# Performance work log

Measured on AMD Instinct MI355X. Metric: run time of the kernel, lower is better.

## Reference

```python
import jax, jax.numpy as jnp
import numpy as np

B, T, C = 4, 1024, 512
H, HD = 8, 64
NE, K = 8, 2
FF = 4 * C


def setup_inputs() -> dict:
    key = jax.random.key(0)
    ks = jax.random.split(key, 16)
    s = 0.02
    return {
        "x": jax.random.normal(ks[0], (B, T, C), jnp.float32),
        "ln1_g": jnp.ones((C,), jnp.float32),
        "ln1_b": jnp.zeros((C,), jnp.float32),
        "ln2_g": jnp.ones((C,), jnp.float32),
        "ln2_b": jnp.zeros((C,), jnp.float32),
        "Wq": jax.random.normal(ks[1], (H, C, HD), jnp.float32) * s,
        "Wk": jax.random.normal(ks[2], (H, C, HD), jnp.float32) * s,
        "Wv": jax.random.normal(ks[3], (H, C, HD), jnp.float32) * s,
        "Wp": jax.random.normal(ks[4], (H * HD, C), jnp.float32) * s,
        "bp": jnp.zeros((C,), jnp.float32),
        "Wr": jax.random.normal(ks[5], (C, NE), jnp.float32) * s,
        "br": jnp.zeros((NE,), jnp.float32),
        "W1": jax.random.normal(ks[6], (NE, C, FF), jnp.float32) * s,
        "b1": jnp.zeros((NE, FF), jnp.float32),
        "W2": jax.random.normal(ks[7], (NE, FF, C), jnp.float32) * s,
        "b2": jnp.zeros((NE, C), jnp.float32),
    }


def _ln(x, g, b, eps=1e-5):
    mu = jnp.mean(x, axis=-1, keepdims=True)
    var = jnp.var(x, axis=-1, keepdims=True)
    return (x - mu) * jax.lax.rsqrt(var + eps) * g + b


def reference(x, ln1_g, ln1_b, ln2_g, ln2_b, Wq, Wk, Wv, Wp, bp, Wr, br, W1, b1, W2, b2):
    # --- multi-head causal attention (all heads stacked) ---
    h = _ln(x, ln1_g, ln1_b)
    q = jnp.einsum("btc,hcd->bhtd", h, Wq)
    k = jnp.einsum("btc,hcd->bhtd", h, Wk)
    v = jnp.einsum("btc,hcd->bhtd", h, Wv)
    wei = jnp.einsum("bhtd,bhsd->bhts", q, k) / np.sqrt(HD).astype(np.float32)
    causal = jnp.tril(jnp.ones((T, T), bool))
    wei = jnp.where(causal, wei, -jnp.inf)
    wei = jax.nn.softmax(wei, axis=-1)
    attn = jnp.einsum("bhts,bhsd->bhtd", wei, v)  # [B,H,T,HD]
    attn = attn.transpose(0, 2, 1, 3).reshape(B, T, H * HD)
    x2 = x + attn @ Wp + bp

    # --- SparseMoE: dense all-experts compute, masked top-k combine ---
    h2 = _ln(x2, ln2_g, ln2_b)
    scores = h2 @ Wr + br  # [B,T,NE]
    topk_scores, indices = jax.lax.top_k(scores, K)
    # scatter top-k scores into zeros (rest stays 0), then softmax over experts
    mask = jnp.sum(jax.nn.one_hot(indices, NE, dtype=scores.dtype) * topk_scores[..., None], axis=-2)
    router = jax.nn.softmax(mask, axis=-1)  # [B,T,NE]
    hid = jax.nn.relu(jnp.einsum("btc,ecf->btef", h2, W1) + b1)  # [B,T,NE,FF]
    eo = jnp.einsum("btef,efc->btec", hid, W2) + b2  # [B,T,NE,C]
    moe = jnp.einsum("bte,btec->btc", router, eo)
    return x2 + moe
```

## Files before the change

kernel.cpp:

```cpp
#include <hip/hip_runtime.h>


typedef unsigned short u16;
typedef __attribute__((ext_vector_type(8))) short s16x8;
typedef __attribute__((ext_vector_type(4))) float f32x4;

__device__ __forceinline__ u16 f2bf(float f) {
  union { float f; unsigned u; } v; v.f = f;
  unsigned r = v.u + 0x7fffu + ((v.u >> 16) & 1u);
  return (u16)(r >> 16);
}
__device__ __forceinline__ float bf2f(u16 h) {
  union { unsigned u; float f; } v; v.u = ((unsigned)h) << 16;
  return v.f;
}

#define GLDS16(g, s) __builtin_amdgcn_global_load_lds( \
    (const __attribute__((address_space(1))) void*)(g), \
    (__attribute__((address_space(3))) void*)(s), 16, 0, 0)

#define MFMA16(a, b, c) __builtin_amdgcn_mfma_f32_16x16x32_bf16((a), (b), (c), 0, 0, 0)

__global__ __launch_bounds__(256) void transpose_k(
    const float* __restrict__ in, u16* __restrict__ out,
    int R, int C, long long ibs, long long obs, float scale)
{
  __shared__ float tile[32][33];
  in  += (long long)blockIdx.z * ibs;
  out += (long long)blockIdx.z * obs;
  const int c0 = blockIdx.x * 32, r0 = blockIdx.y * 32;
  const int tx = threadIdx.x, ty = threadIdx.y;
  #pragma unroll
  for (int i = 0; i < 4; ++i)
    tile[ty + i*8][tx] = in[(size_t)(r0 + ty + i*8) * C + c0 + tx];
  __syncthreads();
  #pragma unroll
  for (int i = 0; i < 4; ++i)
    out[(size_t)(c0 + ty + i*8) * R + r0 + tx] = f2bf(tile[tx][ty + i*8] * scale);
}

__global__ __launch_bounds__(256) void transW_k(
    const float* __restrict__ W1, const float* __restrict__ W2,
    u16* __restrict__ w1t, u16* __restrict__ w2f)
{
  __shared__ float tile[32][33];
  const int z = blockIdx.z;
  const int tx = threadIdx.x, ty = threadIdx.y;
  if (z < 8) {
    const float* in = W1 + (size_t)z * 512 * 2048;
    u16* out = w1t + (size_t)z * 2048 * 512;
    const int c0 = blockIdx.x * 32, r0 = blockIdx.y * 32;
    #pragma unroll
    for (int i = 0; i < 4; ++i)
      tile[ty + i*8][tx] = in[(size_t)(r0 + ty + i*8) * 2048 + c0 + tx];
    __syncthreads();
    #pragma unroll
    for (int i = 0; i < 4; ++i)
      out[(size_t)(c0 + ty + i*8) * 512 + r0 + tx] = f2bf(tile[tx][ty + i*8]);
  } else {
    const int e = z - 8;
    const float* in = W2 + (size_t)e * 2048 * 512;
    const int r0 = blockIdx.x * 32, c0 = blockIdx.y * 32;
    #pragma unroll
    for (int i = 0; i < 4; ++i)
      tile[ty + i*8][tx] = in[(size_t)(r0 + ty + i*8) * 512 + c0 + tx];
    __syncthreads();
    #pragma unroll
    for (int i = 0; i < 4; ++i)
      w2f[(size_t)(c0 + ty + i*8) * 16384 + e*2048 + r0 + tx] = f2bf(tile[tx][ty + i*8]);
  }
}

__global__ __launch_bounds__(256) void transqkv_k(
    const float* __restrict__ Wq, const float* __restrict__ Wk,
    const float* __restrict__ Wv, const float* __restrict__ Wp,
    u16* __restrict__ oqkv, u16* __restrict__ owp)
{
  __shared__ float tile[32][33];
  const int z = blockIdx.z;
  const int tx = threadIdx.x, ty = threadIdx.y;
  if (z < 24) {
    const int which = z >> 3, head = z & 7;
    const float* in = (which == 0 ? Wq : (which == 1 ? Wk : Wv)) + (size_t)head * 512 * 64;
    u16* o = oqkv + (size_t)which * 512 * 512 + (size_t)head * 64 * 512;
    const float scale = (which == 0) ? 0.125f : 1.f;
    const int c0 = blockIdx.x * 32, r0 = blockIdx.y * 32;
    #pragma unroll
    for (int i = 0; i < 4; ++i)
      tile[ty + i*8][tx] = in[(size_t)(r0 + ty + i*8) * 64 + c0 + tx];
    __syncthreads();
    #pragma unroll
    for (int i = 0; i < 4; ++i)
      o[(size_t)(c0 + ty + i*8) * 512 + r0 + tx] = f2bf(tile[tx][ty + i*8] * scale);
  } else {
    const int zz = z - 24;
    const int c0 = (zz * 2 + blockIdx.x) * 32;
    const int r0 = blockIdx.y * 32;
    #pragma unroll
    for (int i = 0; i < 4; ++i)
      tile[ty + i*8][tx] = Wp[(size_t)(r0 + ty + i*8) * 512 + c0 + tx];
    __syncthreads();
    #pragma unroll
    for (int i = 0; i < 4; ++i)
      owp[(size_t)(c0 + ty + i*8) * 512 + r0 + tx] = f2bf(tile[tx][ty + i*8]);
  }
}

__global__ __launch_bounds__(256) void vtrans_k(
    const u16* __restrict__ qkv, u16* __restrict__ vt)
{
  __shared__ u16 tile[32][33];
  const int bh = blockIdx.z, b = bh >> 3, h = bh & 7;
  const int t0 = blockIdx.x * 32, d0 = blockIdx.y * 32;
  const int tx = threadIdx.x, ty = threadIdx.y;
  #pragma unroll
  for (int i = 0; i < 4; ++i)
    tile[ty + i*8][tx] = qkv[(size_t)(b*1024 + t0 + ty + i*8) * 1536 + 1024 + h*64 + d0 + tx];
  __syncthreads();
  #pragma unroll
  for (int i = 0; i < 4; ++i)
    vt[(size_t)bh*65536 + (size_t)(d0 + ty + i*8) * 1024 + t0 + tx] = tile[tx][ty + i*8];
}

__global__ __launch_bounds__(256) void ln_k(
    const float* __restrict__ x, const float* __restrict__ g,
    const float* __restrict__ b, u16* __restrict__ o)
{
  const int row = blockIdx.x, t = threadIdx.x;
  const float* xr = x + (size_t)row * 512;
  const float a0 = xr[t], a1 = xr[t + 256];
  float s = a0 + a1, ss = a0*a0 + a1*a1;
  #pragma unroll
  for (int off = 1; off < 64; off <<= 1) {
    s  += __shfl_xor(s, off);
    ss += __shfl_xor(ss, off);
  }
  __shared__ float rs[4], rq[4];
  const int w = t >> 6;
  if ((t & 63) == 0) { rs[w] = s; rq[w] = ss; }
  __syncthreads();
  s  = rs[0] + rs[1] + rs[2] + rs[3];
  ss = rq[0] + rq[1] + rq[2] + rq[3];
  const float mu = s * (1.f/512.f);
  const float var = ss * (1.f/512.f) - mu*mu;
  const float rstd = rsqrtf(var + 1e-5f);
  o[(size_t)row*512 + t]       = f2bf((a0 - mu) * rstd * g[t]     + b[t]);
  o[(size_t)row*512 + t + 256] = f2bf((a1 - mu) * rstd * g[t+256] + b[t+256]);
}

template<int BN, int EPI>
__global__ __launch_bounds__(256) void gemm2p(
    const u16* __restrict__ A, const u16* __restrict__ Bt,
    int M, int N, int K, int lda, int ldb,
    u16* __restrict__ obf, float* __restrict__ oa,
    const float* __restrict__ bias, const float* __restrict__ extra, int e0)
{
  constexpr int NB = BN / 32;
  constexpr int SB = BN / 32;
  __shared__ u16 Asm[2][128*64];
  __shared__ u16 Bsm[2][BN*64];
  const int t = threadIdx.x, l = t & 63;
  const int wid = t >> 6, wr = wid >> 1, wc = wid & 1;
  const int lrow = l & 15, lhi = l >> 4;
  const int m0 = blockIdx.x * 128, n0 = blockIdx.y * BN;

  const f32x4 z4 = {0.f, 0.f, 0.f, 0.f};
  f32x4 acc[4][NB];
  #pragma unroll
  for (int i = 0; i < 4; ++i)
    #pragma unroll
    for (int j = 0; j < NB; ++j) acc[i][j] = z4;

  const int csw = ((t & 7) ^ ((t >> 3) & 7)) * 8;
  const u16* ga = A  + (size_t)(m0 + (t >> 3)) * lda + csw;
  const u16* gb = Bt + (size_t)(n0 + (t >> 3)) * ldb + csw;

#define STG2(buf, k0) do { \
    _Pragma("unroll") \
    for (int i = 0; i < 4; ++i) \
      GLDS16(ga + (size_t)(i*32)*lda + (k0), (char*)Asm[buf] + i*4096 + t*16); \
    _Pragma("unroll") \
    for (int i = 0; i < SB; ++i) \
      GLDS16(gb + (size_t)(i*32)*ldb + (k0), (char*)Bsm[buf] + i*4096 + t*16); \
  } while (0)

#define RD2(Ls, row, kb) (*(const s16x8*)((const char*)(Ls) + (row)*128 + ((kb) ^ (((row)&7)<<4))))

  const int NT = K >> 6;
  STG2(0, 0);
  for (int tt = 0; tt < NT; ++tt) {
    if (tt + 1 < NT) {
      STG2((tt + 1) & 1, (tt + 1) * 64);
      if constexpr (BN == 128)     asm volatile("s_waitcnt vmcnt(8)" ::: "memory");
      else if constexpr (BN == 96) asm volatile("s_waitcnt vmcnt(7)" ::: "memory");
      else                         asm volatile("s_waitcnt vmcnt(6)" ::: "memory");
    } else {
      asm volatile("s_waitcnt vmcnt(0)" ::: "memory");
    }
    __builtin_amdgcn_sched_barrier(0);
    __builtin_amdgcn_s_barrier();
    const u16* As = Asm[tt & 1];
    const u16* Bs = Bsm[tt & 1];
    #pragma unroll
    for (int kh = 0; kh < 2; ++kh) {
      s16x8 af[4], bfr[NB];
      #pragma unroll
      for (int i = 0; i < 4; ++i)
        af[i]  = RD2(As, wr*64 + i*16 + lrow, kh*64 + lhi*16);
      #pragma unroll
      for (int j = 0; j < NB; ++j)
        bfr[j] = RD2(Bs, wc*(BN/2) + j*16 + lrow, kh*64 + lhi*16);
      #pragma unroll
      for (int i = 0; i < 4; ++i)
        #pragma unroll
        for (int j = 0; j < NB; ++j)
          acc[i][j] = MFMA16(af[i], bfr[j], acc[i][j]);
    }
    __builtin_amdgcn_s_barrier();
    __builtin_amdgcn_sched_barrier(0);
  }
#undef STG2
#undef RD2

  #pragma unroll
  for (int i = 0; i < 4; ++i) {
    const int rbase = m0 + wr*64 + i*16 + lhi*4;
    #pragma unroll
    for (int j = 0; j < NB; ++j) {
      const int col = n0 + wc*(BN/2) + j*16 + lrow;
      #pragma unroll
      for (int rr = 0; rr < 4; ++rr) {
        const int row = rbase + rr;
        const float v = acc[i][j][rr];
        if (EPI == 0) {
          obf[(size_t)row*N + col] = f2bf(v);
        } else if (EPI == 1) {
          const float r = extra[(size_t)row*8 + e0 + (col >> 11)];
          obf[(size_t)row*N + col] = f2bf(fmaxf(v + bias[col], 0.f) * r);
        } else {
          oa[(size_t)row*N + col] = v + bias[col] + extra[(size_t)row*N + col];
        }
      }
    }
  }
}

template<int NKT, int EPI>
__global__ __launch_bounds__(512, 2) void gemm8p(
    const u16* __restrict__ A, const u16* __restrict__ Bt,
    int lda, int ldb,
    u16* __restrict__ obf,
    const float* __restrict__ bias, const float* __restrict__ rout)
{
  __shared__ u16 Lds[2][2][256*64];
  const int t = threadIdx.x, l = t & 63;
  const int wid = t >> 6, wm = wid >> 2, wn = wid & 3;
  const int lrow = l & 15, lhi = l >> 4;

  int m0, n0, zz = 0;
  {
    const int bid = blockIdx.x;
    const int r = bid & 7, k = bid >> 3;
    if (EPI == 1) {
      m0 = (k >> 3) * 256; n0 = (r * 8 + (k & 7)) * 256;
    } else if (EPI == 2) {
      n0 = (r * 8 + (k & 7)) * 256; m0 = (k >> 3) * 256;
    } else if (EPI == 4) {
      zz = r*4 + (k & 3);
      const int mn = k >> 2;
      m0 = (mn >> 1) * 256; n0 = (mn & 1) * 256;
    } else {
      zz = r*2 + (k & 1);
      const int mn = k >> 1;
      m0 = (mn >> 1) * 256; n0 = (mn & 1) * 256;
    }
  }
  constexpr int KCH = (EPI == 4) ? 512 : 1024;
  const u16* Ab = A  + (size_t)m0 * lda + ((EPI == 4 || EPI == 5) ? zz * KCH : 0);
  const u16* Bb = Bt + (size_t)n0 * ldb + ((EPI == 4 || EPI == 5) ? zz * KCH : 0);

  const int tr = t >> 3;
  const int sc = ((t & 7) ^ (tr & 7)) * 8;

#define STGU(bf, kt, op_, u4_) do { \
    const u16* s_ = (op_) ? Bb : Ab; \
    const int ld_ = (op_) ? ldb : lda; \
    GLDS16(s_ + (size_t)((u4_)*64 + tr) * ld_ + (size_t)(kt)*64 + sc, \
           (char*)&Lds[bf][op_][0] + (u4_)*8192 + t*16); \
  } while (0)

#define RD(Ls, row, kb) (*(const s16x8*)((const char*)(Ls) + (row)*128 + ((kb) ^ (((row)&7)<<4))))

  f32x4 acc[8][4];
  const f32x4 z4 = {0.f, 0.f, 0.f, 0.f};
  #pragma unroll
  for (int i = 0; i < 8; ++i)
    #pragma unroll
    for (int j = 0; j < 4; ++j) acc[i][j] = z4;

  #pragma unroll
  for (int u = 0; u < 4; ++u) STGU(0, 0, 0, u);
  #pragma unroll
  for (int u = 0; u < 4; ++u) STGU(0, 0, 1, u);
  if (NKT > 1) {
    #pragma unroll
    for (int u = 0; u < 4; ++u) STGU(1, 1, 1, u);
    asm volatile("s_waitcnt vmcnt(4)" ::: "memory");
  } else {
    asm volatile("s_waitcnt vmcnt(0)" ::: "memory");
  }
  __builtin_amdgcn_sched_barrier(0);
  __builtin_amdgcn_s_barrier();

  s16x8 frA[2][4], frB[2][4];
  #pragma unroll 2
  for (int X = 0; X < NKT; ++X) {
    const u16* As = &Lds[X & 1][0][0];
    const u16* Bs = &Lds[X & 1][1][0];
    #pragma unroll
    for (int kk = 0; kk < 2; ++kk) {
      #pragma unroll
      for (int nf = 0; nf < 4; ++nf)
        frB[kk][nf] = RD(Bs, wn*64 + nf*16 + lrow, kk*64 + lhi*16);
      #pragma unroll
      for (int mf = 0; mf < 4; ++mf)
        frA[kk][mf] = RD(As, wm*128 + mf*16 + lrow, kk*64 + lhi*16);
    }
    if (X + 1 < NKT) {
      #pragma unroll
      for (int u = 0; u < 4; ++u) STGU((X + 1) & 1, X + 1, 0, u);
    }
    __builtin_amdgcn_s_barrier();
    asm volatile("s_waitcnt lgkmcnt(0)" ::: "memory");
    __builtin_amdgcn_sched_barrier(0);
    __builtin_amdgcn_s_setprio(1);
    #pragma unroll
    for (int kk = 0; kk < 2; ++kk)
      #pragma unroll
      for (int mf = 0; mf < 4; ++mf)
        #pragma unroll
        for (int nf = 0; nf < 4; ++nf)
          acc[mf][nf] = MFMA16(frA[kk][mf], frB[kk][nf], acc[mf][nf]);
    __builtin_amdgcn_s_setprio(0);
    __builtin_amdgcn_s_barrier();
    #pragma unroll
    for (int kk = 0; kk < 2; ++kk)
      #pragma unroll
      for (int mf = 0; mf < 4; ++mf)
        frA[kk][mf] = RD(As, wm*128 + 64 + mf*16 + lrow, kk*64 + lhi*16);
    if (X + 2 < NKT) {
      #pragma unroll
      for (int u = 0; u < 4; ++u) STGU(X & 1, X + 2, 1, u);
    }
    __builtin_amdgcn_s_barrier();
    asm volatile("s_waitcnt lgkmcnt(0)" ::: "memory");
    __builtin_amdgcn_sched_barrier(0);
    __builtin_amdgcn_s_setprio(1);
    #pragma unroll
    for (int kk = 0; kk < 2; ++kk)
      #pragma unroll
      for (int mf = 0; mf < 4; ++mf)
        #pragma unroll
        for (int nf = 0; nf < 4; ++nf)
          acc[4 + mf][nf] = MFMA16(frA[kk][mf], frB[kk][nf], acc[4 + mf][nf]);
    __builtin_amdgcn_s_setprio(0);
    if (X + 1 < NKT) {
      if (X + 2 < NKT) asm volatile("s_waitcnt vmcnt(4)" ::: "memory");
      else             asm volatile("s_waitcnt vmcnt(0)" ::: "memory");
      __builtin_amdgcn_sched_barrier(0);
    }
    __builtin_amdgcn_s_barrier();
  }
#undef STGU
#undef RD

  constexpr size_t PSTRIDE = (EPI == 4) ? (size_t)1024*512 : (size_t)2048*512;
  u16* outp = (EPI == 4 || EPI == 5) ? obf + (size_t)zz * PSTRIDE : obf;
  #pragma unroll
  for (int mf = 0; mf < 8; ++mf) {
    const int rbase = m0 + wm*128 + mf*16 + lhi*4;
    #pragma unroll
    for (int nf = 0; nf < 4; ++nf) {
      const int col = n0 + wn*64 + nf*16 + lrow;
      #pragma unroll
      for (int rr = 0; rr < 4; ++rr) {
        const int row = rbase + rr;
        float v = acc[mf][nf][rr];
        if (EPI == 1 || EPI == 2) {
          const float r = rout[(size_t)row*8 + (col >> 11)];
          outp[(size_t)row*16384 + col] = f2bf(fmaxf(v + bias[col], 0.f) * r);
        } else {
          outp[(size_t)row*512 + col] = f2bf(v);
        }
      }
    }
  }
}

template<int Z>
__global__ __launch_bounds__(256) void combineZ_k(
    float* __restrict__ outq, const u16* __restrict__ P, size_t pstride,
    const float* __restrict__ routq, const float* __restrict__ b2)
{
  const int row = blockIdx.x, t = threadIdx.x;
  const int c = t * 2;
  float r[8];
  #pragma unroll
  for (int e = 0; e < 8; ++e) r[e] = routq[(size_t)row*8 + e];
  float v0 = outq[(size_t)row*512 + c];
  float v1 = outq[(size_t)row*512 + c + 1];
  #pragma unroll
  for (int z = 0; z < Z; ++z) {
    const unsigned pv = *(const unsigned*)(P + (size_t)z*pstride + (size_t)row*512 + c);
    v0 += bf2f((u16)(pv & 0xffffu));
    v1 += bf2f((u16)(pv >> 16));
  }
  #pragma unroll
  for (int e = 0; e < 8; ++e) {
    v0 += r[e] * b2[(size_t)e*512 + c];
    v1 += r[e] * b2[(size_t)e*512 + c + 1];
  }
  outq[(size_t)row*512 + c]     = v0;
  outq[(size_t)row*512 + c + 1] = v1;
}

__global__ __launch_bounds__(256) void gemm2_k(
    const u16* __restrict__ hid, const u16* __restrict__ w2t,
    u16* __restrict__ P, int e0, int accum)
{
  __shared__ u16 Asm[128*64];
  __shared__ u16 Bsm[64*64];
  const int t = threadIdx.x;
  const int l = t & 63;
  const int wid = t >> 6, wr = wid >> 1, wc = wid & 1;
  const int lrow = l & 15, lhi = l >> 4;
  const int m0 = blockIdx.x * 128, n0 = blockIdx.y * 64, z = blockIdx.z;

  const u16* A  = hid + z * 2048;
  const u16* Bt = w2t + (size_t)(e0 + z) * 512 * 2048;
  u16* Pz = P + (size_t)z * 4096 * 512;

  const f32x4 z4 = {0.f, 0.f, 0.f, 0.f};
  f32x4 acc[4][2];
  #pragma unroll
  for (int i = 0; i < 4; ++i) { acc[i][0] = z4; acc[i][1] = z4; }

  const u16* ga = A  + (size_t)(m0 + (t >> 3)) * 4096 + (t & 7) * 8;
  const u16* gb = Bt + (size_t)(n0 + (t >> 3)) * 2048 + (t & 7) * 8;

  for (int k0 = 0; k0 < 2048; k0 += 64) {
    #pragma unroll
    for (int i = 0; i < 4; ++i)
      GLDS16(ga + (size_t)i*32*4096 + k0, (char*)Asm + i*4096 + t*16);
    #pragma unroll
    for (int i = 0; i < 2; ++i)
      GLDS16(gb + (size_t)i*32*2048 + k0, (char*)Bsm + i*4096 + t*16);
    __syncthreads();
    #pragma unroll
    for (int kh = 0; kh < 2; ++kh) {
      s16x8 af[4], bfr[2];
      #pragma unroll
      for (int i = 0; i < 4; ++i)
        af[i]  = *(const s16x8*)(Asm + (wr*64 + i*16 + lrow)*64 + kh*32 + lhi*8);
      #pragma unroll
      for (int j = 0; j < 2; ++j)
        bfr[j] = *(const s16x8*)(Bsm + (wc*32 + j*16 + lrow)*64 + kh*32 + lhi*8);
      #pragma unroll
      for (int i = 0; i < 4; ++i)
        #pragma unroll
        for (int j = 0; j < 2; ++j)
          acc[i][j] = MFMA16(af[i], bfr[j], acc[i][j]);
    }
    __syncthreads();
  }

  #pragma unroll
  for (int i = 0; i < 4; ++i) {
    const int rbase = m0 + wr*64 + i*16 + lhi*4;
    #pragma unroll
    for (int j = 0; j < 2; ++j) {
      const int col = n0 + wc*32 + j*16 + lrow;
      #pragma unroll
      for (int rr = 0; rr < 4; ++rr) {
        const size_t idx = (size_t)(rbase + rr) * 512 + col;
        const float old = accum ? bf2f(Pz[idx]) : 0.f;
        Pz[idx] = f2bf(old + acc[i][j][rr]);
      }
    }
  }
}

__global__ __launch_bounds__(256) void combineB_k(
    float* __restrict__ out, const u16* __restrict__ P,
    const float* __restrict__ rout, const float* __restrict__ b2)
{
  const int row = blockIdx.x, t = threadIdx.x;
  float r[8];
  #pragma unroll
  for (int e = 0; e < 8; ++e) r[e] = rout[(size_t)row*8 + e];
  #pragma unroll
  for (int cc = 0; cc < 2; ++cc) {
    const int c = t + cc*256;
    const size_t idx = (size_t)row*512 + c;
    float v = out[idx] + bf2f(P[idx]) + bf2f(P[(size_t)4096*512 + idx]);
    #pragma unroll
    for (int e = 0; e < 8; ++e) v += r[e] * b2[(size_t)e*512 + c];
    out[idx] = v;
  }
}

__global__ __launch_bounds__(256) void attn_k(
    const u16* __restrict__ qkv, const u16* __restrict__ vt, u16* __restrict__ o)
{
  const int bid = blockIdx.x;
  const int xcd = bid & 7, rr_ = bid >> 3;
  const int bh = (rr_ >> 3) * 8 + xcd;
  const int qp = rr_ & 7;
  const int b = bh >> 3, h = bh & 7;
  const int t = threadIdx.x, l = t & 63, w = t >> 6;
  const int lrow = l & 15, lhi = l >> 4;

  __shared__ u16 Ksm[2][128*64];
  __shared__ u16 Vsm[2][64*128];
  __shared__ u16 Psm[4][16][136];

  const int trow = t >> 3;
  const int csw = ((t & 7) ^ (trow & 7)) * 8;
  const int vrow = t >> 4;
  const int vsw = ((t & 15) ^ (vrow & 7)) * 8;
  const u16* gk = qkv + (size_t)(b*1024 + trow) * 1536 + 512 + h*64 + csw;
  const u16* gv = vt + (size_t)bh*65536 + (size_t)vrow*1024 + vsw;
  const f32x4 z4 = {0.f,0.f,0.f,0.f};

#define ASTAGE(buf, s0) do { \
    _Pragma("unroll") \
    for (int i = 0; i < 4; ++i) \
      GLDS16(gk + (size_t)((s0) + i*32) * 1536, (char*)Ksm[buf] + i*4096 + t*16); \
    _Pragma("unroll") \
    for (int i = 0; i < 4; ++i) \
      GLDS16(gv + (s0) + (size_t)(i*16)*1024,   (char*)Vsm[buf] + i*4096 + t*16); \
  } while (0)

  for (int pass = 0; pass < 2; ++pass) {
    const int qb = pass ? (15 - qp) : qp;
    const int t0w = qb*64 + w*16;
    const u16* qrow = qkv + (size_t)(b*1024 + t0w + lrow) * 1536 + h*64 + lhi*8;
    s16x8 qf0 = *(const s16x8*)qrow;
    s16x8 qf1 = *(const s16x8*)(qrow + 32);

    float m[4], sl[4];
    f32x4 oacc[4];
    #pragma unroll
    for (int i = 0; i < 4; ++i) { m[i] = -1e30f; sl[i] = 0.f; oacc[i] = z4; }

    const int nt = (qb >> 1) + 1;
    ASTAGE(0, 0);
    for (int kv = 0; kv < nt; ++kv) {
      const int s0 = kv * 128;
      if (kv + 1 < nt) {
        ASTAGE((kv + 1) & 1, s0 + 128);
        asm volatile("s_waitcnt vmcnt(8)" ::: "memory");
      } else {
        asm volatile("s_waitcnt vmcnt(0)" ::: "memory");
      }
      __builtin_amdgcn_s_barrier();
      __builtin_amdgcn_sched_barrier(0);
      const u16* Ks = Ksm[kv & 1];
      const u16* Vs = Vsm[kv & 1];

      f32x4 sacc[8];
      #pragma unroll
      for (int n = 0; n < 8; ++n) sacc[n] = z4;
      #pragma unroll
      for (int n = 0; n < 8; ++n) {
        const int r = n*16 + lrow;
        s16x8 kf0 = *(const s16x8*)((const char*)Ks + r*128 + ((lhi*16) ^ ((r & 7) << 4)));
        s16x8 kf1 = *(const s16x8*)((const char*)Ks + r*128 + ((64 + lhi*16) ^ ((r & 7) << 4)));
        sacc[n] = MFMA16(qf0, kf0, sacc[n]);
        sacc[n] = MFMA16(qf1, kf1, sacc[n]);
      }
      if (s0 + 127 > t0w) {
        #pragma unroll
        for (int n = 0; n < 8; ++n)
          #pragma unroll
          for (int rr = 0; rr < 4; ++rr)
            if (s0 + n*16 + lrow > t0w + lhi*4 + rr) sacc[n][rr] = -1e30f;
      }
      float pm[4];
      #pragma unroll
      for (int rr = 0; rr < 4; ++rr) {
        float a = fmaxf(fmaxf(sacc[0][rr], sacc[1][rr]), fmaxf(sacc[2][rr], sacc[3][rr]));
        float bmx = fmaxf(fmaxf(sacc[4][rr], sacc[5][rr]), fmaxf(sacc[6][rr], sacc[7][rr]));
        pm[rr] = fmaxf(a, bmx);
      }
      #pragma unroll
      for (int rr = 0; rr < 4; ++rr) {
        pm[rr] = fmaxf(pm[rr], __shfl_xor(pm[rr], 1));
        pm[rr] = fmaxf(pm[rr], __shfl_xor(pm[rr], 2));
        pm[rr] = fmaxf(pm[rr], __shfl_xor(pm[rr], 4));
        pm[rr] = fmaxf(pm[rr], __shfl_xor(pm[rr], 8));
      }
      float p[8][4], ps[4], scv[4];
      #pragma unroll
      for (int rr = 0; rr < 4; ++rr) {
        const float mn = fmaxf(m[rr], pm[rr]);
        scv[rr] = __expf(m[rr] - mn);
        m[rr] = mn;
        ps[rr] = 0.f;
        #pragma unroll
        for (int n = 0; n < 8; ++n) {
          p[n][rr] = __expf(sacc[n][rr] - mn);
          ps[rr] += p[n][rr];
        }
      }
      #pragma unroll
      for (int rr = 0; rr < 4; ++rr) {
        ps[rr] += __shfl_xor(ps[rr], 1);
        ps[rr] += __shfl_xor(ps[rr], 2);
        ps[rr] += __shfl_xor(ps[rr], 4);
        ps[rr] += __shfl_xor(ps[rr], 8);
        sl[rr] = sl[rr] * scv[rr] + ps[rr];
      }
      #pragma unroll
      for (int ct = 0; ct < 4; ++ct) {
        f32x4 t4 = oacc[ct];
        #pragma unroll
        for (int rr = 0; rr < 4; ++rr) t4[rr] *= scv[rr];
        oacc[ct] = t4;
      }
      #pragma unroll
      for (int n = 0; n < 8; ++n)
        #pragma unroll
        for (int rr = 0; rr < 4; ++rr)
          Psm[w][lhi*4 + rr][n*16 + lrow] = f2bf(p[n][rr]);
      asm volatile("s_waitcnt lgkmcnt(0)" ::: "memory");
      __builtin_amdgcn_sched_barrier(0);
      s16x8 pa[4];
      #pragma unroll
      for (int s = 0; s < 4; ++s)
        pa[s] = *(const s16x8*)&Psm[w][lrow][s*32 + lhi*8];
      #pragma unroll
      for (int ct = 0; ct < 4; ++ct) {
        const int r = ct*16 + lrow;
        #pragma unroll
        for (int s = 0; s < 4; ++s) {
          s16x8 vb = *(const s16x8*)((const char*)Vs + r*256 + ((s*64 + lhi*16) ^ ((r & 7) << 4)));
          oacc[ct] = MFMA16(pa[s], vb, oacc[ct]);
        }
      }
      __builtin_amdgcn_s_barrier();
      __builtin_amdgcn_sched_barrier(0);
    }
    #pragma unroll
    for (int ct = 0; ct < 4; ++ct)
      #pragma unroll
      for (int rr = 0; rr < 4; ++rr) {
        const int row = b*1024 + t0w + lhi*4 + rr;
        o[(size_t)row*512 + h*64 + ct*16 + lrow] = f2bf(oacc[ct][rr] / sl[rr]);
      }
  }
#undef ASTAGE
}

__global__ __launch_bounds__(256) void router_k(
    const float* __restrict__ x2, const float* __restrict__ g,
    const float* __restrict__ b, const float* __restrict__ Wr,
    const float* __restrict__ br, float* __restrict__ rt,
    u16* __restrict__ h2o)
{
  const int l = threadIdx.x & 63, w = threadIdx.x >> 6;
  const int tkn = blockIdx.x * 4 + w;
  const float* xr = x2 + (size_t)tkn * 512;
  float v[8];
  float s = 0.f, ss = 0.f;
  #pragma unroll
  for (int i = 0; i < 8; ++i) {
    v[i] = xr[l*8 + i];
    s += v[i]; ss += v[i]*v[i];
  }
  #pragma unroll
  for (int off = 1; off < 64; off <<= 1) {
    s  += __shfl_xor(s, off);
    ss += __shfl_xor(ss, off);
  }
  const float mu = s * (1.f/512.f);
  const float var = ss * (1.f/512.f) - mu*mu;
  const float rstd = rsqrtf(var + 1e-5f);
  float acc[8];
  #pragma unroll
  for (int e = 0; e < 8; ++e) acc[e] = 0.f;
  s16x8 hw;
  #pragma unroll
  for (int i = 0; i < 8; ++i) {
    const int c = l*8 + i;
    const float hv = (v[i] - mu) * rstd * g[c] + b[c];
    hw[i] = (short)f2bf(hv);
    const float* wrow = Wr + (size_t)c * 8;
    #pragma unroll
    for (int e = 0; e < 8; ++e) acc[e] += hv * wrow[e];
  }
  *(s16x8*)(h2o + (size_t)tkn*512 + l*8) = hw;
  #pragma unroll
  for (int e = 0; e < 8; ++e) {
    #pragma unroll
    for (int off = 1; off < 64; off <<= 1) acc[e] += __shfl_xor(acc[e], off);
    acc[e] += br[e];
  }
  int e1 = 0;
  #pragma unroll
  for (int e = 1; e < 8; ++e) if (acc[e] > acc[e1]) e1 = e;
  int e2 = (e1 == 0) ? 1 : 0;
  #pragma unroll
  for (int e = 0; e < 8; ++e) if (e != e1 && acc[e] > acc[e2]) e2 = e;
  const float mx = fmaxf(acc[e1], 0.f);
  float Z = 0.f;
  #pragma unroll
  for (int e = 0; e < 8; ++e) {
    const float mv = (e == e1 || e == e2) ? acc[e] : 0.f;
    Z += __expf(mv - mx);
  }
  if (l < 8) {
    const float mv = (l == e1 || l == e2) ? acc[l] : 0.f;
    rt[(size_t)tkn * 8 + l] = __expf(mv - mx) / Z;
  }
}

extern "C" void kernel_launch(void* const* d_in, const int* in_sizes, int n_in,
                              void* d_out, int out_size, void* d_ws, size_t ws_size,
                              hipStream_t stream) {
  const float* x    = (const float*)d_in[0];
  const float* ln1g = (const float*)d_in[1];
  const float* ln1b = (const float*)d_in[2];
  const float* ln2g = (const float*)d_in[3];
  const float* ln2b = (const float*)d_in[4];
  const float* Wq   = (const float*)d_in[5];
  const float* Wk   = (const float*)d_in[6];
  const float* Wv   = (const float*)d_in[7];
  const float* Wp   = (const float*)d_in[8];
  const float* bp   = (const float*)d_in[9];
  const float* Wr   = (const float*)d_in[10];
  const float* br   = (const float*)d_in[11];
  const float* W1   = (const float*)d_in[12];
  const float* b1   = (const float*)d_in[13];
  const float* W2   = (const float*)d_in[14];
  const float* b2   = (const float*)d_in[15];
  float* out = (float*)d_out;

  const int pathH = (ws_size >= (size_t)138543104) ? 1 : 0;
  const int pathN = (ws_size >= (size_t)104988672) ? 1 : 0;

  char* ws = (char*)d_ws;
  size_t off = 0;
  auto alloc = [&](size_t bytes) -> char* {
    char* p = ws + off;
    off += (bytes + 255) & ~(size_t)255;
    return p;
  };
  u16* w1_t = (u16*)alloc((size_t)8*2048*512*2);
  u16* w2f  = (u16*)alloc((size_t)8*512*2048*2);
  u16* h2b  = (u16*)alloc((size_t)4096*512*2);
  float* rout = (float*)alloc((size_t)4096*8*4);
  u16* hidq = (u16*)alloc(pathH ? (size_t)2048*16384*2 : (size_t)4096*4096*2);
  u16* Ppl  = (u16*)alloc(pathH ? (size_t)16*2048*512*2
                                : (pathN ? (size_t)32*1024*512*2 : (size_t)2*4096*512*2));
  u16* wqkv_t = (u16*)hidq;
  u16* wp_t   = (u16*)((char*)hidq + 1572864);
  u16* hb     = (u16*)((char*)hidq + 2097152);
  u16* attnb  = (u16*)((char*)hidq + 6291456);
  u16* qkvb   = (u16*)((char*)hidq + 10485760);
  u16* vtb    = (u16*)((char*)hidq + 23068672);

  const dim3 tb(32, 8);
  transqkv_k<<<dim3(2,16,32), tb, 0, stream>>>(Wq, Wk, Wv, Wp, wqkv_t, wp_t);
  if (pathN) {
    transW_k<<<dim3(64,16,16), tb, 0, stream>>>(W1, W2, w1_t, w2f);
  } else {
    transpose_k<<<dim3(64,16,8), tb, 0, stream>>>(W1, w1_t, 512, 2048,
        (long long)512*2048, (long long)2048*512, 1.f);
    transpose_k<<<dim3(16,64,8), tb, 0, stream>>>(W2, w2f, 2048, 512,
        (long long)2048*512, (long long)512*2048, 1.f);
  }

  ln_k<<<4096, 256, 0, stream>>>(x, ln1g, ln1b, hb);
  gemm2p<96,0><<<dim3(32,16), 256, 0, stream>>>(hb, wqkv_t, 4096, 1536, 512, 512, 512,
                                                qkvb, nullptr, nullptr, nullptr, 0);
  vtrans_k<<<dim3(32,2,32), tb, 0, stream>>>(qkvb, vtb);
  attn_k<<<256, 256, 0, stream>>>(qkvb, vtb, attnb);
  gemm2p<64,2><<<dim3(32,8), 256, 0, stream>>>(attnb, wp_t, 4096, 512, 512, 512, 512,
                                               nullptr, out, bp, x, 0);
  router_k<<<1024, 256, 0, stream>>>(out, ln2g, ln2b, Wr, br, rout, h2b);

  if (pathH) {
    for (int h = 0; h < 2; ++h) {
      gemm8p<8,2><<<512, 512, 0, stream>>>(h2b + (size_t)h*2048*512, w1_t, 512, 512,
                                           hidq, b1, rout + (size_t)h*16384);
      gemm8p<16,5><<<256, 512, 0, stream>>>(hidq, w2f, 16384, 16384,
                                            Ppl, nullptr, nullptr);
      combineZ_k<16><<<2048, 256, 0, stream>>>(out + (size_t)h*2048*512, Ppl,
                                               (size_t)2048*512,
                                               rout + (size_t)h*16384, b2);
    }
  } else if (pathN) {
    for (int q = 0; q < 4; ++q) {
      gemm8p<8,1><<<256, 512, 0, stream>>>(h2b + (size_t)q*1024*512, w1_t, 512, 512,
                                           hidq, b1, rout + (size_t)q*8192);
      gemm8p<8,4><<<256, 512, 0, stream>>>(hidq, w2f, 16384, 16384,
                                           Ppl, nullptr, nullptr);
      combineZ_k<32><<<1024, 256, 0, stream>>>(out + (size_t)q*1024*512, Ppl,
                                               (size_t)1024*512,
                                               rout + (size_t)q*8192, b2);
    }
  } else {
    for (int p = 0; p < 4; ++p) {
      const int e0 = 2*p;
      gemm2p<128,1><<<dim3(32,32), 256, 0, stream>>>(h2b, w1_t + (size_t)e0*2048*512,
                                                     4096, 4096, 512, 512, 512,
                                                     hidq, nullptr, b1 + (size_t)e0*2048, rout, e0);
      gemm2_k<<<dim3(32,8,2), 256, 0, stream>>>(hidq, w2f, Ppl, e0, p > 0 ? 1 : 0);
    }
    combineB_k<<<4096, 256, 0, stream>>>(out, Ppl, rout, b2);
  }
}
```

Measured before the change: 268.0 us.

## Replace MoE first-layer GEMM with single-stage 256x64 tile kernel

Adds a new GEMM kernel for the expert W1 projection in the half-batch path. It uses 256x64 output tiles, one LDS buffer with an XOR swizzle, and direct global-to-LDS loads. The epilogue fuses bias, ReLU and router-weight scaling. The kernel waits for all loads before computing, with no double buffering, which trades load/compute overlap for a simpler launch shape of 2048 blocks of 256 threads. Blocks are interleaved across experts by block index.

```diff
diff --git a/kernel.cpp b/kernel.cpp
--- a/kernel.cpp
+++ b/kernel.cpp
@@ -146,6 +146,81 @@
   const float rstd = rsqrtf(var + 1e-5f);
   o[(size_t)row*512 + t]       = f2bf((a0 - mu) * rstd * g[t]     + b[t]);
   o[(size_t)row*512 + t + 256] = f2bf((a1 - mu) * rstd * g[t+256] + b[t+256]);
+}
+
+__global__ __launch_bounds__(256) void gemm1s(
+    const u16* __restrict__ A, const u16* __restrict__ Bt,
+    u16* __restrict__ obf, const float* __restrict__ bias,
+    const float* __restrict__ rout)
+{
+  __shared__ u16 Asm[256*64];
+  __shared__ u16 Bsm[64*64];
+  const int t = threadIdx.x, l = t & 63, wid = t >> 6;
+  const int lrow = l & 15, lhi = l >> 4;
+
+  const int r8 = blockIdx.x & 7, j = blockIdx.x >> 3;
+  const int n0 = r8 * 2048 + (j & 31) * 64;
+  const int m0 = (j >> 5) * 256;
+
+  const f32x4 z4 = {0.f, 0.f, 0.f, 0.f};
+  f32x4 acc[4][4];
+  #pragma unroll
+  for (int i = 0; i < 4; ++i)
+    #pragma unroll
+    for (int jj = 0; jj < 4; ++jj) acc[i][jj] = z4;
+
+  const int tr = t >> 3;
+  const int csw = ((t & 7) ^ (tr & 7)) * 8;
+  const u16* ga = A  + (size_t)(m0 + tr) * 512 + csw;
+  const u16* gb = Bt + (size_t)(n0 + tr) * 512 + csw;
+
+#define RD1(Ls, row, kb) (*(const s16x8*)((const char*)(Ls) + (row)*128 + ((kb) ^ (((row)&7)<<4))))
+
+  for (int k0 = 0; k0 < 512; k0 += 64) {
+    #pragma unroll
+    for (int i = 0; i < 8; ++i)
+      GLDS16(ga + (size_t)(i*32)*512 + k0, (char*)Asm + i*4096 + t*16);
+    #pragma unroll
+    for (int i = 0; i < 2; ++i)
+      GLDS16(gb + (size_t)(i*32)*512 + k0, (char*)Bsm + i*4096 + t*16);
+    asm volatile("s_waitcnt vmcnt(0)" ::: "memory");
+    __builtin_amdgcn_sched_barrier(0);
+    __builtin_amdgcn_s_barrier();
+    #pragma unroll
+    for (int kh = 0; kh < 2; ++kh) {
+      s16x8 af[4], bfr[4];
+      #pragma unroll
+      for (int i = 0; i < 4; ++i)
+        af[i]  = RD1(Asm, wid*64 + i*16 + lrow, kh*64 + lhi*16);
+      #pragma unroll
+      for (int jj = 0; jj < 4; ++jj)
+        bfr[jj] = RD1(Bsm, jj*16 + lrow, kh*64 + lhi*16);
+      #pragma unroll
+      for (int i = 0; i < 4; ++i)
+        #pragma unroll
+        for (int jj = 0; jj < 4; ++jj)
+          acc[i][jj] = MFMA16(af[i], bfr[jj], acc[i][jj]);
+    }
+    __builtin_amdgcn_s_barrier();
+    __builtin_amdgcn_sched_barrier(0);
+  }
+#undef RD1
+
+  #pragma unroll
+  for (int i = 0; i < 4; ++i) {
+    const int rbase = m0 + wid*64 + i*16 + lhi*4;
+    #pragma unroll
+    for (int jj = 0; jj < 4; ++jj) {
+      const int col = n0 + jj*16 + lrow;
+      #pragma unroll
+      for (int rr = 0; rr < 4; ++rr) {
+        const int row = rbase + rr;
+        const float r = rout[(size_t)row*8 + (col >> 11)];
+        obf[(size_t)row*16384 + col] =
+            f2bf(fmaxf(acc[i][jj][rr] + bias[col], 0.f) * r);
+      }
+    }
+  }
 }
 
 template<int BN, int EPI>
@@ -792,8 +867,8 @@
 
   if (pathH) {
     for (int h = 0; h < 2; ++h) {
-      gemm8p<8,2><<<512, 512, 0, stream>>>(h2b + (size_t)h*2048*512, w1_t, 512, 512,
-                                           hidq, b1, rout + (size_t)h*16384);
+      gemm1s<<<2048, 256, 0, stream>>>(h2b + (size_t)h*2048*512, w1_t,
+                                       hidq, b1, rout + (size_t)h*16384);
       gemm8p<16,5><<<256, 512, 0, stream>>>(hidq, w2f, 16384, 16384,
                                             Ppl, nullptr, nullptr);
       combineZ_k<16><<<2048, 256, 0, stream>>>(out + (size_t)h*2048*512, Ppl,
```

After: 276.3 us. 1.03x slower.
